# Kernel tuning notes

Measured on AMD Instinct MI355X. Metric: run time of the kernel, lower is better.

The kernel has to match this reference:

```python
import jax, jax.numpy as jnp
import numpy as np

L, B, D = 4096, 4, 512  # seq_len, batch, embed_dim (nhead=1 so kdim=vdim=D)


def setup_inputs() -> dict:
    key = jax.random.key(0)
    ks = jax.random.split(key, 11)
    sc = 1.0 / np.sqrt(D)
    return {
        "x": jax.random.normal(ks[0], (L, B, D), jnp.float32),
        "e": jax.random.normal(ks[1], (L, B, D), jnp.float32),
        "relay": jax.random.normal(ks[2], (1, B, D), jnp.float32),
        "Wq": jax.random.normal(ks[3], (D, D), jnp.float32) * sc,
        "bq": jax.random.normal(ks[4], (D,), jnp.float32) * sc,
        "Wk": jax.random.normal(ks[5], (D, D), jnp.float32) * sc,
        "bk": jax.random.normal(ks[6], (D,), jnp.float32) * sc,
        "Wv": jax.random.normal(ks[7], (D, D), jnp.float32) * sc,
        "bv": jax.random.normal(ks[8], (D,), jnp.float32) * sc,
        "Wo": jax.random.normal(ks[9], (D, D), jnp.float32) * sc,
        "bo": jax.random.normal(ks[10], (D,), jnp.float32) * sc,
    }


def _window3(t):
    # t: [L,B,D] -> [L,B,3,D] with zero padding at the sequence boundaries
    # (matches nn.Unfold(kernel=[3,1], padding=[1,0]): positions l-1, l, l+1)
    n = t.shape[0]
    tp = jnp.pad(t, ((1, 1), (0, 0), (0, 0)))
    return jnp.stack([tp[:n], tp[1:n + 1], tp[2:n + 2]], axis=2)


def reference(x, e, relay, Wq, bq, Wk, bk, Wv, bv, Wo, bo):
    l, b, d = x.shape
    scale = 1.0 / jnp.sqrt(jnp.asarray(d, x.dtype))

    q = x @ Wq.T + bq          # [L,B,D]
    k = x @ Wk.T + bk
    v = x @ Wv.T + bv

    # cores = [embedding tokens e ; relay broadcast over L]  -> [2,L,B,D]
    s = jnp.broadcast_to(relay, (l, b, d))
    cores = jnp.stack([e, s], axis=0)
    k_c = cores @ Wk.T + bk    # [2,L,B,D]
    v_c = cores @ Wv.T + bv

    # ring (local windowed) attention: window = [k_{l-1},k_l,k_{l+1}, k(e_l), k(relay)]
    kw = jnp.concatenate([_window3(k), jnp.transpose(k_c, (1, 2, 0, 3))], axis=2)  # [L,B,5,D]
    vw = jnp.concatenate([_window3(v), jnp.transpose(v_c, (1, 2, 0, 3))], axis=2)  # [L,B,5,D]
    logits = jnp.einsum('lbd,lbwd->lbw', q, kw) * scale
    alphas = jax.nn.softmax(logits, axis=2)
    ring = jnp.einsum('lbw,lbwd->lbd', alphas, vw)  # [L,B,D]

    # star (relay) attention: query is the UNprojected relay token (as in source)
    k_r = relay @ Wk.T + bk    # [1,B,D]
    v_r = relay @ Wv.T + bv
    kk = jnp.concatenate([k, k_r], axis=0)  # [L+1,B,D]
    vv = jnp.concatenate([v, v_r], axis=0)
    s_logits = jnp.einsum('obd,nbd->bon', relay, kk) * scale  # [B,1,L+1]
    s_alphas = jax.nn.softmax(s_logits, axis=-1)
    star = jnp.einsum('bon,nbd->obd', s_alphas, vv)  # [1,B,D]

    return (ring @ Wo.T + bo, star @ Wo.T + bo)
```

## Files before the change

### kernel.cpp

```cpp
#include <hip/hip_runtime.h>
#include <hip/hip_fp16.h>

#define L_SEQ 4096
#define BATCH 4
#define DIM 512
#define M_ROWS (L_SEQ * BATCH)
#define SCALE 0.04419417382415922f
#define SLS 4097

typedef __attribute__((ext_vector_type(4))) float f32x4;
typedef __attribute__((ext_vector_type(8))) _Float16 f16x8;
typedef __attribute__((ext_vector_type(4))) _Float16 f16x4;

__device__ inline void gload16(const void* g, void* l) {
    __builtin_amdgcn_global_load_lds(
        (const __attribute__((address_space(1))) void*)g,
        (__attribute__((address_space(3))) void*)l, 16, 0, 0);
}

__device__ inline float wred_sum(float s) {
#pragma unroll
    for (int o = 32; o; o >>= 1) s += __shfl_xor(s, o);
    return s;
}
__device__ inline float wred_max(float s) {
#pragma unroll
    for (int o = 32; o; o >>= 1) s = fmaxf(s, __shfl_xor(s, o));
    return s;
}

__global__ __launch_bounds__(256) void prep(
    const float* __restrict__ Wq, const float* __restrict__ Wk,
    const float* __restrict__ Wv, const float* __restrict__ Wo,
    const float* __restrict__ bq, const float* __restrict__ bk, const float* __restrict__ bv,
    const float* __restrict__ relay,
    _Float16* __restrict__ Wqkv, _Float16* __restrict__ Wof, float* __restrict__ bqkv,
    float* __restrict__ krvr, float* __restrict__ star)
{
    const int bid = blockIdx.x;
    if (bid < 768) {
        const int w = bid * 256 + threadIdx.x;
        const int o = w * 4, r = o >> 9, c = o & 511;
        const float* W = (r < 512) ? Wq : (r < 1024 ? Wk : Wv);
        float4 v = *(const float4*)(W + (size_t)(r & 511) * 512 + c);
        *(f16x4*)(Wqkv + o) = f16x4{ (_Float16)v.x, (_Float16)v.y, (_Float16)v.z, (_Float16)v.w };
        if (o < 262144) {
            float4 u = *(const float4*)(Wo + o);
            *(f16x4*)(Wof + o) = f16x4{ (_Float16)u.x, (_Float16)u.y, (_Float16)u.z, (_Float16)u.w };
        }
        if (w < 1536) bqkv[w] = (w < 512) ? bq[w] : (w < 1024 ? bk[w - 512] : bv[w - 1024]);
    } else {
        const int o = ((bid - 768) << 2) + (threadIdx.x >> 6);
        const int lane = threadIdx.x & 63;
        const int sel = o >> 11, rem = o & 2047, b = rem >> 9, j = rem & 511;
        const float* W = sel ? Wv : Wk;
        const float* wr = W + (size_t)j * 512 + lane * 8;
        const float* rp = relay + (size_t)b * 512 + lane * 8;
        float4 w0 = *(const float4*)wr,  w1 = *(const float4*)(wr + 4);
        float4 r0 = *(const float4*)rp,  r1 = *(const float4*)(rp + 4);
        float s = w0.x * r0.x + w0.y * r0.y + w0.z * r0.z + w0.w * r0.w
                + w1.x * r1.x + w1.y * r1.y + w1.z * r1.z + w1.w * r1.w;
        s = wred_sum(s);
        if (lane == 0) {
            krvr[o] = s + (sel ? bv[j] : bk[j]);
            if (o < 2048) star[o] = 0.f;
        }
    }
}

struct GemmP {
    const void*     A;
    const _Float16* W;
    const float*    bias;
    void*           C;
    int             cstride;
    int             ncols;
};

template<int OUT16>
__global__ __launch_bounds__(256) void gemm2p(GemmP g0, GemmP g1, int n0, int cpx)
{
    __shared__ __align__(16) char smem[49152];
    _Float16* lAb = (_Float16*)smem;
    _Float16* lBb = (_Float16*)(smem + 24576);

    const int bid = blockIdx.x;
    const int swz = (bid & 7) * cpx + (bid >> 3);
    const GemmP g = (swz < n0) ? g0 : g1;
    const int l  = (swz < n0) ? swz : swz - n0;
    const int mt = l / g.ncols, nt = l % g.ncols;
    const int row0 = mt * 128, col0 = nt * 128;

    const int tid = threadIdx.x;
    const int wave = tid >> 6, lane = tid & 63;
    const int wm = (wave >> 1) * 64, wn = (wave & 1) * 64;
    const float* Af = (const float*)g.A;

    f32x4 acc[4][4];
#pragma unroll
    for (int i = 0; i < 4; ++i)
#pragma unroll
        for (int j = 0; j < 4; ++j) acc[i][j] = (f32x4)0.f;

    const int idx1 = 256 + tid;
    const int r0_ = tid >> 2,  c0_ = ((tid & 3) ^ ((tid >> 3) & 3)) * 8;
    const int r1_ = idx1 >> 2, c1_ = ((idx1 & 3) ^ ((idx1 >> 3) & 3)) * 8;
    const int ldsb0 = (wave * 64) * 8;
    const int ldsb1 = (256 + wave * 64) * 8;

    auto stageB = [&](int slot, int t) {
        const int k0 = t << 5;
        gload16(g.W + (size_t)(col0 + r0_) * 512 + k0 + c0_, lBb + slot * 4096 + ldsb0);
        gload16(g.W + (size_t)(col0 + r1_) * 512 + k0 + c1_, lBb + slot * 4096 + ldsb1);
    };
    f32x4 a0[4], a1[4], a2[4];
    auto loadA = [&](f32x4* d, int t) {
        const int k0 = t << 5;
        const float* p0 = Af + (size_t)(row0 + r0_) * 512 + k0 + c0_;
        const float* p1 = Af + (size_t)(row0 + r1_) * 512 + k0 + c1_;
        d[0] = *(const f32x4*)p0; d[1] = *(const f32x4*)(p0 + 4);
        d[2] = *(const f32x4*)p1; d[3] = *(const f32x4*)(p1 + 4);
    };
    auto writeA = [&](const f32x4* s, int slot) {
        f16x8 h0 = { (_Float16)s[0][0], (_Float16)s[0][1], (_Float16)s[0][2], (_Float16)s[0][3],
                     (_Float16)s[1][0], (_Float16)s[1][1], (_Float16)s[1][2], (_Float16)s[1][3] };
        f16x8 h1 = { (_Float16)s[2][0], (_Float16)s[2][1], (_Float16)s[2][2], (_Float16)s[2][3],
                     (_Float16)s[3][0], (_Float16)s[3][1], (_Float16)s[3][2], (_Float16)s[3][3] };
        *(f16x8*)(lAb + slot * 4096 + tid * 8) = h0;
        *(f16x8*)(lAb + slot * 4096 + (256 + tid) * 8) = h1;
    };

    stageB(0, 0); stageB(1, 1); stageB(2, 2);
    asm volatile("" ::: "memory");
    loadA(a0, 0); asm volatile("" ::: "memory");
    loadA(a1, 1); asm volatile("" ::: "memory");
    loadA(a2, 2);
    asm volatile("s_waitcnt vmcnt(8)" ::: "memory");
    writeA(a0, 0);
    asm volatile("s_waitcnt lgkmcnt(0)" ::: "memory");

    const int rslot = ((lane >> 4) ^ ((lane >> 1) & 3)) * 8;
    const int arb = (wm + (lane & 15)) * 32 + rslot;
    const int brb = (wn + (lane & 15)) * 32 + rslot;

    auto step = [&](int t, int slot, int swrt, f32x4* aW, f32x4* aL) {
        if (t == 0)      asm volatile("s_waitcnt vmcnt(4)" ::: "memory");
        else if (t < 14) asm volatile("s_waitcnt vmcnt(6)" ::: "memory");
        else             asm volatile("s_waitcnt vmcnt(0)" ::: "memory");
        __builtin_amdgcn_s_barrier();
        f16x8 af[4], bfr[4];
#pragma unroll
        for (int i = 0; i < 4; ++i) af[i]  = *(const f16x8*)(lAb + slot * 4096 + arb + i * 512);
#pragma unroll
        for (int i = 0; i < 4; ++i) bfr[i] = *(const f16x8*)(lBb + slot * 4096 + brb + i * 512);
        __builtin_amdgcn_s_setprio(1);
#pragma unroll
        for (int mi = 0; mi < 4; ++mi)
#pragma unroll
            for (int ni = 0; ni < 4; ++ni)
                acc[mi][ni] = __builtin_amdgcn_mfma_f32_16x16x32_f16(
                    af[mi], bfr[ni], acc[mi][ni], 0, 0, 0);
        __builtin_amdgcn_s_setprio(0);
        if (t < 15) writeA(aW, swrt);
        asm volatile("s_waitcnt lgkmcnt(0)" ::: "memory");
        __builtin_amdgcn_s_barrier();
        if (t <= 12) {
            stageB(slot, t + 3);
            asm volatile("" ::: "memory");
            loadA(aL, t + 3);
        }
    };
#pragma unroll 1
    for (int tb = 0; tb < 15; tb += 3) {
        step(tb,     0, 1, a1, a0);
        step(tb + 1, 1, 2, a2, a1);
        step(tb + 2, 2, 0, a0, a2);
    }
    step(15, 0, 1, a1, a0);

    const int h = lane >> 4, c = lane & 15;
    if (OUT16) {
        _Float16* ep = (_Float16*)smem;
#pragma unroll
        for (int mi = 0; mi < 4; ++mi)
#pragma unroll
            for (int ni = 0; ni < 4; ++ni) {
                const float bb = g.bias[col0 + wn + ni * 16 + c];
#pragma unroll
                for (int r = 0; r < 4; ++r)
                    ep[(wm + mi * 16 + h * 4 + r) * 136 + wn + ni * 16 + c] =
                        (_Float16)(acc[mi][ni][r] + bb);
            }
        __syncthreads();
        const int rt = tid >> 4, ct = (tid & 15) * 8;
#pragma unroll
        for (int j = 0; j < 8; ++j) {
            const int row = j * 16 + rt;
            f16x8 v = *(const f16x8*)(ep + row * 136 + ct);
            *(f16x8*)((_Float16*)g.C + (size_t)(row0 + row) * g.cstride + col0 + ct) = v;
        }
    } else {
        float* ep = (float*)smem;
#pragma unroll
        for (int pass = 0; pass < 2; ++pass) {
            if ((wm == 0) == (pass == 0)) {
#pragma unroll
                for (int mi = 0; mi < 4; ++mi)
#pragma unroll
                    for (int ni = 0; ni < 4; ++ni) {
                        const float bb = g.bias[col0 + wn + ni * 16 + c];
#pragma unroll
                        for (int r = 0; r < 4; ++r)
                            ep[(mi * 16 + h * 4 + r) * 132 + wn + ni * 16 + c] =
                                acc[mi][ni][r] + bb;
                    }
            }
            __syncthreads();
            const int rt = tid >> 5, ct4 = (tid & 31) * 4;
#pragma unroll
            for (int j = 0; j < 8; ++j) {
                const int row = j * 8 + rt;
                f32x4 v = *(const f32x4*)(ep + row * 132 + ct4);
                *(f32x4*)((float*)g.C + (size_t)(row0 + pass * 64 + row) * g.cstride + col0 + ct4) = v;
            }
            if (pass == 0) __syncthreads();
        }
    }
}

__global__ __launch_bounds__(256) void tail_fused(GemmP g,
    const float* __restrict__ star, const float* __restrict__ Wo,
    const float* __restrict__ bo, float* __restrict__ out1)
{
    __shared__ __align__(16) char smem[49152];
    const int bid = blockIdx.x;
    const int tid = threadIdx.x;
    const int lane = tid & 63;

    if (bid >= 512) {
        const int o = ((bid - 512) << 2) + (tid >> 6);
        const int b = o >> 9, j = o & 511;
        const float* sp = star + (size_t)b * 512 + lane * 8;
        const float* wr = Wo + (size_t)j * 512 + lane * 8;
        float4 w0 = *(const float4*)wr,  w1 = *(const float4*)(wr + 4);
        float4 s0 = *(const float4*)sp,  s1 = *(const float4*)(sp + 4);
        float s = w0.x * s0.x + w0.y * s0.y + w0.z * s0.z + w0.w * s0.w
                + w1.x * s1.x + w1.y * s1.y + w1.z * s1.z + w1.w * s1.w;
        s = wred_sum(s);
        if (lane == 0) out1[o] = s + bo[j];
        return;
    }

    _Float16* lAb = (_Float16*)smem;
    _Float16* lBb = (_Float16*)(smem + 24576);
    const _Float16* Ah = (const _Float16*)g.A;

    const int swz = (bid & 7) * 64 + (bid >> 3);
    const int mt = swz / g.ncols, nt = swz % g.ncols;
    const int row0 = mt * 128, col0 = nt * 128;

    const int wave = tid >> 6;
    const int wm = (wave >> 1) * 64, wn = (wave & 1) * 64;

    f32x4 acc[4][4];
#pragma unroll
    for (int i = 0; i < 4; ++i)
#pragma unroll
        for (int j = 0; j < 4; ++j) acc[i][j] = (f32x4)0.f;

    const int idx0 = tid, idx1 = 256 + tid;
    const int r0_ = idx0 >> 2, c0_ = ((idx0 & 3) ^ ((idx0 >> 3) & 3)) * 8;
    const int r1_ = idx1 >> 2, c1_ = ((idx1 & 3) ^ ((idx1 >> 3) & 3)) * 8;
    const int ldsb0 = (wave * 64) * 8;
    const int ldsb1 = (256 + wave * 64) * 8;

    auto stage = [&](int buf, int t) {
        const int k0 = t << 5;
        gload16(Ah + (size_t)(row0 + r0_) * 512 + k0 + c0_, lAb + buf * 4096 + ldsb0);
        gload16(Ah + (size_t)(row0 + r1_) * 512 + k0 + c1_, lAb + buf * 4096 + ldsb1);
        gload16(g.W + (size_t)(col0 + r0_) * 512 + k0 + c0_, lBb + buf * 4096 + ldsb0);
        gload16(g.W + (size_t)(col0 + r1_) * 512 + k0 + c1_, lBb + buf * 4096 + ldsb1);
    };
    stage(0, 0);
    stage(1, 1);
    stage(2, 2);

    const int rslot = ((lane >> 4) ^ ((lane >> 1) & 3)) * 8;
    const int arb = (wm + (lane & 15)) * 32 + rslot;
    const int brb = (wn + (lane & 15)) * 32 + rslot;

    int rs = 0;
#pragma unroll 1
    for (int t = 0; t < 16; ++t) {
        if (t < 14)       asm volatile("s_waitcnt vmcnt(8)" ::: "memory");
        else if (t == 14) asm volatile("s_waitcnt vmcnt(4)" ::: "memory");
        else              asm volatile("s_waitcnt vmcnt(0)" ::: "memory");
        __builtin_amdgcn_s_barrier();
        f16x8 af[4], bfr[4];
#pragma unroll
        for (int i = 0; i < 4; ++i) af[i]  = *(const f16x8*)(lAb + rs * 4096 + arb + i * 512);
#pragma unroll
        for (int i = 0; i < 4; ++i) bfr[i] = *(const f16x8*)(lBb + rs * 4096 + brb + i * 512);
        __builtin_amdgcn_s_setprio(1);
#pragma unroll
        for (int mi = 0; mi < 4; ++mi)
#pragma unroll
            for (int ni = 0; ni < 4; ++ni)
                acc[mi][ni] = __builtin_amdgcn_mfma_f32_16x16x32_f16(
                    af[mi], bfr[ni], acc[mi][ni], 0, 0, 0);
        __builtin_amdgcn_s_setprio(0);
        asm volatile("s_waitcnt lgkmcnt(0)" ::: "memory");
        __builtin_amdgcn_s_barrier();
        if (t + 3 < 16) stage(rs, t + 3);
        rs = (rs == 2) ? 0 : rs + 1;
    }

    const int h = lane >> 4, c = lane & 15;
    float* ep = (float*)smem;
#pragma unroll
    for (int pass = 0; pass < 2; ++pass) {
        if ((wm == 0) == (pass == 0)) {
#pragma unroll
            for (int mi = 0; mi < 4; ++mi)
#pragma unroll
                for (int ni = 0; ni < 4; ++ni) {
                    const float bb = g.bias[col0 + wn + ni * 16 + c];
#pragma unroll
                    for (int r = 0; r < 4; ++r)
                        ep[(mi * 16 + h * 4 + r) * 132 + wn + ni * 16 + c] =
                            acc[mi][ni][r] + bb;
                }
        }
        __syncthreads();
        const int rt = tid >> 5, ct4 = (tid & 31) * 4;
#pragma unroll
        for (int j = 0; j < 8; ++j) {
            const int row = j * 8 + rt;
            f32x4 v = *(const f32x4*)(ep + row * 132 + ct4);
            *(f32x4*)((float*)g.C + (size_t)(row0 + pass * 64 + row) * g.cstride + col0 + ct4) = v;
        }
        if (pass == 0) __syncthreads();
    }
}

__global__ __launch_bounds__(256) void ring_attn(
    const _Float16* __restrict__ qkv,
    const _Float16* __restrict__ ekv,
    const float* __restrict__ krvr,
    const float* __restrict__ relay,
    _Float16* __restrict__ ring,
    float* __restrict__ slog)
{
    const int wid = (blockIdx.x << 2) + (threadIdx.x >> 6);
    const int lane = threadIdx.x & 63;
    const int r = wid, b = r & 3, l = r >> 2;
    const int d0 = lane << 3;

    float q[8], rl[8];
    {
        f16x8 t = *(const f16x8*)(qkv + (size_t)r * 1536 + d0);
#pragma unroll
        for (int i = 0; i < 8; ++i) q[i] = (float)t[i];
        const float* rp = relay + (size_t)b * 512 + d0;
        float4 a = *(const float4*)rp, c = *(const float4*)(rp + 4);
        rl[0] = a.x; rl[1] = a.y; rl[2] = a.z; rl[3] = a.w;
        rl[4] = c.x; rl[5] = c.y; rl[6] = c.z; rl[7] = c.w;
    }
    const bool has0 = (l > 0), has2 = (l < L_SEQ - 1);

    auto dotk = [&](const _Float16* kp) -> float {
        f16x8 t = *(const f16x8*)(kp + d0);
        float s = 0.f;
#pragma unroll
        for (int i = 0; i < 8; ++i) s += q[i] * (float)t[i];
        return wred_sum(s);
    };

    float lg[5];
    lg[0] = has0 ? dotk(qkv + (size_t)(r - 4) * 1536 + 512) : 0.f;
    lg[2] = has2 ? dotk(qkv + (size_t)(r + 4) * 1536 + 512) : 0.f;
    lg[3] = dotk(ekv + (size_t)r * 1024);
    {
        f16x8 t = *(const f16x8*)(qkv + (size_t)r * 1536 + 512 + d0);
        float s1 = 0.f, s2 = 0.f;
#pragma unroll
        for (int i = 0; i < 8; ++i) { float kf = (float)t[i]; s1 += q[i] * kf; s2 += rl[i] * kf; }
#pragma unroll
        for (int o = 32; o; o >>= 1) { s1 += __shfl_xor(s1, o); s2 += __shfl_xor(s2, o); }
        lg[1] = s1;
        if (lane == 0) slog[(size_t)b * SLS + l] = s2 * SCALE;
    }
    {
        const float* kp = krvr + (size_t)b * 512 + d0;
        float s = 0.f;
#pragma unroll
        for (int i = 0; i < 8; ++i) s += q[i] * kp[i];
        lg[4] = wred_sum(s);
    }

    float li[5], m = -1e30f;
#pragma unroll
    for (int w = 0; w < 5; ++w) { li[w] = lg[w] * SCALE; m = fmaxf(m, li[w]); }
    float ew[5], Z = 0.f;
#pragma unroll
    for (int w = 0; w < 5; ++w) { ew[w] = expf(li[w] - m); Z += ew[w]; }
    const float inv = 1.f / Z;

    float o8[8] = {0, 0, 0, 0, 0, 0, 0, 0};
    auto addv = [&](const _Float16* vp, float a) {
        f16x8 t = *(const f16x8*)(vp + d0);
#pragma unroll
        for (int i = 0; i < 8; ++i) o8[i] += a * (float)t[i];
    };
    if (has0) addv(qkv + (size_t)(r - 4) * 1536 + 1024, ew[0] * inv);
    addv(qkv + (size_t)r * 1536 + 1024, ew[1] * inv);
    if (has2) addv(qkv + (size_t)(r + 4) * 1536 + 1024, ew[2] * inv);
    addv(ekv + (size_t)r * 1024 + 512, ew[3] * inv);
    {
        const float* vp = krvr + 2048 + (size_t)b * 512 + d0;
        const float a = ew[4] * inv;
#pragma unroll
        for (int i = 0; i < 8; ++i) o8[i] += a * vp[i];
    }
    f16x8 res;
#pragma unroll
    for (int i = 0; i < 8; ++i) res[i] = (_Float16)o8[i];
    *(f16x8*)(ring + (size_t)r * 512 + d0) = res;
}

__global__ __launch_bounds__(1024) void star_softmax(
    const float* __restrict__ relay, const float* __restrict__ krvr,
    float* __restrict__ slog)
{
    const int b = blockIdx.x, t = threadIdx.x, lane = t & 63, w = t >> 6;
    __shared__ float red[16];
    __shared__ float bc[2];
    float* sl = slog + (size_t)b * SLS;

    float p = 0.f;
    if (t < 512) p = relay[(size_t)b * 512 + t] * krvr[(size_t)b * 512 + t];
    p = wred_sum(p);
    if (lane == 0) red[w] = p;
    __syncthreads();
    if (t == 0) { float s = 0.f; for (int i = 0; i < 16; ++i) s += red[i]; bc[0] = s * SCALE; }
    __syncthreads();
    const float selfl = bc[0];
    __syncthreads();

    float v[4];
#pragma unroll
    for (int i = 0; i < 4; ++i) v[i] = sl[t + i * 1024];

    float m = selfl;
#pragma unroll
    for (int i = 0; i < 4; ++i) m = fmaxf(m, v[i]);
    m = wred_max(m);
    if (lane == 0) red[w] = m;
    __syncthreads();
    if (t == 0) { float mm = red[0]; for (int i = 1; i < 16; ++i) mm = fmaxf(mm, red[i]); bc[1] = mm; }
    __syncthreads();
    m = bc[1];

    float ev[4], z = (t == 0) ? expf(selfl - m) : 0.f;
#pragma unroll
    for (int i = 0; i < 4; ++i) { ev[i] = expf(v[i] - m); z += ev[i]; }
    z = wred_sum(z);
    if (lane == 0) red[w] = z;
    __syncthreads();
    if (t == 0) { float s = 0.f; for (int i = 0; i < 16; ++i) s += red[i]; bc[0] = 1.f / s; }
    __syncthreads();
    const float inv = bc[0];

#pragma unroll
    for (int i = 0; i < 4; ++i) sl[t + i * 1024] = ev[i] * inv;
    if (t == 0) sl[SLS - 1] = expf(selfl - m) * inv;
}

__global__ __launch_bounds__(256) void star_out(
    const float* __restrict__ slog, const _Float16* __restrict__ qkv,
    const float* __restrict__ krvr, float* __restrict__ star)
{
    const int b = threadIdx.x >> 6, lane = threadIdx.x & 63;
    const int chunk = blockIdx.x;
    const int d0 = lane << 3;
    const float* al = slog + (size_t)b * SLS;
    float acc[8] = {0, 0, 0, 0, 0, 0, 0, 0};
#pragma unroll 4
    for (int i = 0; i < 64; ++i) {
        const int n = chunk * 64 + i;
        const float a = al[n];
        f16x8 v = *(const f16x8*)(qkv + (size_t)(n * 4 + b) * 1536 + 1024 + d0);
#pragma unroll
        for (int j = 0; j < 8; ++j) acc[j] += a * (float)v[j];
    }
    if (chunk == 63) {
        const float a = al[SLS - 1];
        const float* vr = krvr + 2048 + (size_t)b * 512 + d0;
#pragma unroll
        for (int j = 0; j < 8; ++j) acc[j] += a * vr[j];
    }
#pragma unroll
    for (int j = 0; j < 8; ++j) atomicAdd(&star[(size_t)b * 512 + d0 + j], acc[j]);
}

extern "C" void kernel_launch(void* const* d_in, const int* in_sizes, int n_in,
                              void* d_out, int out_size, void* d_ws, size_t ws_size,
                              hipStream_t stream) {
    const float* x     = (const float*)d_in[0];
    const float* e     = (const float*)d_in[1];
    const float* relay = (const float*)d_in[2];
    const float* Wq    = (const float*)d_in[3];
    const float* bq    = (const float*)d_in[4];
    const float* Wk    = (const float*)d_in[5];
    const float* bk    = (const float*)d_in[6];
    const float* Wv    = (const float*)d_in[7];
    const float* bv    = (const float*)d_in[8];
    const float* Wo    = (const float*)d_in[9];
    const float* bo    = (const float*)d_in[10];
    float* out = (float*)d_out;

    size_t off = 0;
    auto alloc = [&](size_t bytes) {
        void* p = (char*)d_ws + off;
        off += (bytes + 255) & ~(size_t)255;
        return p;
    };
    _Float16* Wqkv = (_Float16*)alloc((size_t)1536 * 512 * 2);
    _Float16* Wof  = (_Float16*)alloc((size_t)512 * 512 * 2);
    float*    bqkv = (float*)   alloc(1536 * 4);
    _Float16* qkv  = (_Float16*)alloc((size_t)M_ROWS * 1536 * 2);
    _Float16* ekv  = (_Float16*)alloc((size_t)M_ROWS * 1024 * 2);
    _Float16* ringb= (_Float16*)alloc((size_t)M_ROWS * 512 * 2);
    float*    krvr = (float*)   alloc(2 * 4 * 512 * 4);
    float*    slog = (float*)   alloc((size_t)4 * SLS * 4);
    float*    star = (float*)   alloc(4 * 512 * 4);

    prep<<<768 + 1024, 256, 0, stream>>>(
        Wq, Wk, Wv, Wo, bq, bk, bv, relay,
        Wqkv, Wof, bqkv, krvr, star);

    GemmP gq { x, Wqkv,                     bqkv,       qkv, 1536, 12 };
    GemmP ge { e, Wqkv + (size_t)512 * 512, bqkv + 512, ekv, 1024,  8 };
    gemm2p<1><<<2560, 256, 0, stream>>>(gq, ge, 1536, 320);

    ring_attn<<<M_ROWS / 4, 256, 0, stream>>>(qkv, ekv, krvr, relay, ringb, slog);

    star_softmax<<<4, 1024, 0, stream>>>(relay, krvr, slog);
    star_out<<<64, 256, 0, stream>>>(slog, qkv, krvr, star);

    GemmP go { ringb, Wof, bo, out, 512, 4 };
    tail_fused<<<1024, 256, 0, stream>>>(go, star, Wo, bo, out + (size_t)M_ROWS * 512);
}
```

Measured before the change: 149.4 us.

## Stage fp32 A tiles directly into LDS via async loads, convert at fragment read

The GEMM previously loaded fp32 A tiles into registers, converted them to fp16 and wrote them to LDS, while B was loaded asynchronously with global_load_lds. Now A is also staged as fp32 straight into LDS through async direct-to-LDS loads with an XOR swizzle, and the fp32-to-fp16 conversion happens when each wave reads its MFMA fragments. This removes the register round-trip and the explicit LDS write from the pipeline and simplifies it into a uniform triple-buffered loop. In exchange LDS use rises from 48KB to 72KB per block, which may lower occupancy, and every wave now repeats the conversion and reads twice as many A bytes from LDS.

```diff
diff --git a/kernel.cpp b/kernel.cpp
--- a/kernel.cpp
+++ b/kernel.cpp
@@ -80,9 +80,9 @@
 template<int OUT16>
 __global__ __launch_bounds__(256) void gemm2p(GemmP g0, GemmP g1, int n0, int cpx)
 {
-    __shared__ __align__(16) char smem[49152];
-    _Float16* lAb = (_Float16*)smem;
-    _Float16* lBb = (_Float16*)(smem + 24576);
+    __shared__ __align__(16) char smem[73728];
+    float*    sAf = (float*)smem;
+    _Float16* sBh = (_Float16*)(smem + 49152);
 
     const int bid = blockIdx.x;
     const int swz = (bid & 7) * cpx + (bid >> 3);
@@ -102,57 +102,52 @@
 #pragma unroll
         for (int j = 0; j < 4; ++j) acc[i][j] = (f32x4)0.f;
 
+    const int arow  = tid >> 3;
+    const int aslot = (tid & 7) ^ ((tid >> 3) & 7);
     const int idx1 = 256 + tid;
-    const int r0_ = tid >> 2,  c0_ = ((tid & 3) ^ ((tid >> 3) & 3)) * 8;
-    const int r1_ = idx1 >> 2, c1_ = ((idx1 & 3) ^ ((idx1 >> 3) & 3)) * 8;
+    const int br0 = tid >> 2,  bc0 = ((tid & 3) ^ ((tid >> 3) & 3)) * 8;
+    const int br1 = idx1 >> 2, bc1 = ((idx1 & 3) ^ ((idx1 >> 3) & 3)) * 8;
     const int ldsb0 = (wave * 64) * 8;
     const int ldsb1 = (256 + wave * 64) * 8;
 
-    auto stageB = [&](int slot, int t) {
+    auto stage = [&](int buf, int t) {
         const int k0 = t << 5;
-        gload16(g.W + (size_t)(col0 + r0_) * 512 + k0 + c0_, lBb + slot * 4096 + ldsb0);
-        gload16(g.W + (size_t)(col0 + r1_) * 512 + k0 + c1_, lBb + slot * 4096 + ldsb1);
+        const float* As = Af + (size_t)row0 * 512 + k0 + aslot * 4;
+#pragma unroll
+        for (int r = 0; r < 4; ++r)
+            gload16(As + (size_t)(r * 32 + arow) * 512,
+                    sAf + buf * 4096 + (r * 256 + wave * 64) * 4);
+        gload16(g.W + (size_t)(col0 + br0) * 512 + k0 + bc0, sBh + buf * 4096 + ldsb0);
+        gload16(g.W + (size_t)(col0 + br1) * 512 + k0 + bc1, sBh + buf * 4096 + ldsb1);
     };
-    f32x4 a0[4], a1[4], a2[4];
-    auto loadA = [&](f32x4* d, int t) {
-        const int k0 = t << 5;
-        const float* p0 = Af + (size_t)(row0 + r0_) * 512 + k0 + c0_;
-        const float* p1 = Af + (size_t)(row0 + r1_) * 512 + k0 + c1_;
-        d[0] = *(const f32x4*)p0; d[1] = *(const f32x4*)(p0 + 4);
-        d[2] = *(const f32x4*)p1; d[3] = *(const f32x4*)(p1 + 4);
-    };
-    auto writeA = [&](const f32x4* s, int slot) {
-        f16x8 h0 = { (_Float16)s[0][0], (_Float16)s[0][1], (_Float16)s[0][2], (_Float16)s[0][3],
-                     (_Float16)s[1][0], (_Float16)s[1][1], (_Float16)s[1][2], (_Float16)s[1][3] };
-        f16x8 h1 = { (_Float16)s[2][0], (_Float16)s[2][1], (_Float16)s[2][2], (_Float16)s[2][3],
-                     (_Float16)s[3][0], (_Float16)s[3][1], (_Float16)s[3][2], (_Float16)s[3][3] };
-        *(f16x8*)(lAb + slot * 4096 + tid * 8) = h0;
-        *(f16x8*)(lAb + slot * 4096 + (256 + tid) * 8) = h1;
-    };
-
-    stageB(0, 0); stageB(1, 1); stageB(2, 2);
-    asm volatile("" ::: "memory");
-    loadA(a0, 0); asm volatile("" ::: "memory");
-    loadA(a1, 1); asm volatile("" ::: "memory");
-    loadA(a2, 2);
-    asm volatile("s_waitcnt vmcnt(8)" ::: "memory");
-    writeA(a0, 0);
-    asm volatile("s_waitcnt lgkmcnt(0)" ::: "memory");
-
+    stage(0, 0);
+    stage(1, 1);
+    stage(2, 2);
+
+    const int aq0 = (((lane >> 4) * 2) ^ (lane & 7)) * 4;
+    const int aq1 = ((((lane >> 4) * 2) + 1) ^ (lane & 7)) * 4;
+    const int arbase = (wm + (lane & 15)) * 32;
     const int rslot = ((lane >> 4) ^ ((lane >> 1) & 3)) * 8;
-    const int arb = (wm + (lane & 15)) * 32 + rslot;
     const int brb = (wn + (lane & 15)) * 32 + rslot;
 
-    auto step = [&](int t, int slot, int swrt, f32x4* aW, f32x4* aL) {
-        if (t == 0)      asm volatile("s_waitcnt vmcnt(4)" ::: "memory");
-        else if (t < 14) asm volatile("s_waitcnt vmcnt(6)" ::: "memory");
-        else             asm volatile("s_waitcnt vmcnt(0)" ::: "memory");
+    int rs = 0;
+#pragma unroll 1
+    for (int t = 0; t < 16; ++t) {
+        if (t < 14)       asm volatile("s_waitcnt vmcnt(12)" ::: "memory");
+        else if (t == 14) asm volatile("s_waitcnt vmcnt(6)"  ::: "memory");
+        else              asm volatile("s_waitcnt vmcnt(0)"  ::: "memory");
         __builtin_amdgcn_s_barrier();
+        const float* pa = sAf + rs * 4096 + arbase;
         f16x8 af[4], bfr[4];
 #pragma unroll
-        for (int i = 0; i < 4; ++i) af[i]  = *(const f16x8*)(lAb + slot * 4096 + arb + i * 512);
-#pragma unroll
-        for (int i = 0; i < 4; ++i) bfr[i] = *(const f16x8*)(lBb + slot * 4096 + brb + i * 512);
+        for (int i = 0; i < 4; ++i) bfr[i] = *(const f16x8*)(sBh + rs * 4096 + brb + i * 512);
+#pragma unroll
+        for (int mi = 0; mi < 4; ++mi) {
+            f32x4 u = *(const f32x4*)(pa + mi * 512 + aq0);
+            f32x4 v = *(const f32x4*)(pa + mi * 512 + aq1);
+            af[mi] = f16x8{ (_Float16)u[0], (_Float16)u[1], (_Float16)u[2], (_Float16)u[3],
+                            (_Float16)v[0], (_Float16)v[1], (_Float16)v[2], (_Float16)v[3] };
+        }
         __builtin_amdgcn_s_setprio(1);
 #pragma unroll
         for (int mi = 0; mi < 4; ++mi)
@@ -161,22 +156,11 @@
                 acc[mi][ni] = __builtin_amdgcn_mfma_f32_16x16x32_f16(
                     af[mi], bfr[ni], acc[mi][ni], 0, 0, 0);
         __builtin_amdgcn_s_setprio(0);
-        if (t < 15) writeA(aW, swrt);
         asm volatile("s_waitcnt lgkmcnt(0)" ::: "memory");
         __builtin_amdgcn_s_barrier();
-        if (t <= 12) {
-            stageB(slot, t + 3);
-            asm volatile("" ::: "memory");
-            loadA(aL, t + 3);
-        }
-    };
-#pragma unroll 1
-    for (int tb = 0; tb < 15; tb += 3) {
-        step(tb,     0, 1, a1, a0);
-        step(tb + 1, 1, 2, a2, a1);
-        step(tb + 2, 2, 0, a0, a2);
-    }
-    step(15, 0, 1, a1, a0);
+        if (t + 3 < 16) stage(rs, t + 3);
+        rs = (rs == 2) ? 0 : rs + 1;
+    }
 
     const int h = lane >> 4, c = lane & 15;
     if (OUT16) {
```

Result: no change. 151.1 us (+1.1%).
